# Optimization experiments

Hardware: AMD Instinct MI355X
Metric: run time of the kernel (lower is better)

The kernel has to match this reference:

```python
import jax, jax.numpy as jnp
import numpy as np

DIM = 64  # per-head dim; temperature init = sqrt(DIM)
B, H, S, D = 4, 12, 2048, 64


def setup_inputs() -> dict:
    key = jax.random.key(0)
    kq, kk, kv = jax.random.split(key, 3)
    Q = jax.random.normal(kq, (B, H, S, D), dtype=jnp.float32)
    K = jax.random.normal(kk, (B, H, S, D), dtype=jnp.float32)
    V = jax.random.normal(kv, (B, H, S, D), dtype=jnp.float32)
    temperature = jnp.ones((1,), dtype=jnp.float32) * (DIM ** 0.5)
    return {"Q": Q, "K": K, "V": V, "temperature": temperature}


def reference(Q, K, V, temperature):
    # scores: [B,H,S,S]
    scores = jnp.einsum("bhqd,bhkd->bhqk", Q, K) / temperature
    s = scores.shape[-1]
    eye = jnp.eye(s, dtype=bool)  # diagonal self-exclusion
    scores = jnp.where(eye, -jnp.inf, scores)
    attn = jax.nn.softmax(scores, axis=-1)
    return jnp.einsum("bhqk,bhkd->bhqd", attn, V)
```

## Files before the change

kernel.cpp:

```cpp
#include <hip/hip_runtime.h>
#include <hip/hip_bf16.h>

#define S_LEN 2048
#define D_DIM 64
#define NHEADS 48
#define QT 128
#define KT 64
#define NKT (S_LEN / KT)
#define HEAD_ELEMS ((size_t)S_LEN * D_DIM)
#define WS_NEED (3ull * NHEADS * S_LEN * D_DIM * 2ull)

typedef short bf16x8 __attribute__((ext_vector_type(8)));
typedef float f32x4 __attribute__((ext_vector_type(4)));

__device__ __forceinline__ unsigned short f2bf(float x) {
    unsigned u = __builtin_bit_cast(unsigned, x);
    u = (u + 0x7fffu + ((u >> 16) & 1u)) >> 16;
    return (unsigned short)u;
}

__device__ __forceinline__ unsigned cvtpk(float lo, float hi) {
    unsigned r;
    asm("v_cvt_pk_bf16_f32 %0, %1, %2" : "=v"(r) : "v"(lo), "v"(hi));
    return r;
}

__device__ __forceinline__ void gload16(const void* g, void* l) {
    __builtin_amdgcn_global_load_lds(
        (const __attribute__((address_space(1))) unsigned int*)g,
        (__attribute__((address_space(3))) unsigned int*)l, 16, 0, 0);
}

__global__ __launch_bounds__(256) void lsa_prep(
    const float* __restrict__ Qg, const float* __restrict__ Kg,
    const float* __restrict__ Vg, const float* __restrict__ Tg,
    unsigned short* __restrict__ Qs, unsigned short* __restrict__ Kf,
    unsigned short* __restrict__ Vf) {
    const int b   = blockIdx.x;
    const int tid = threadIdx.x;
    const int r   = tid >> 4;
    const int c4  = (tid & 15) * 4;

    __shared__ __align__(16) unsigned short Kl[4096];
    __shared__ __align__(16) unsigned short Vl[4096];

    const size_t ibase = (size_t)b * 4096;
    const float qscale = 1.442695041f / Tg[0];

#pragma unroll
    for (int it = 0; it < 4; ++it) {
        const int rr = it * 16 + r;
        const size_t off = ibase + (size_t)rr * D_DIM + c4;

        float4 q4 = *(const float4*)(Qg + off);
        uint2 qo;
        qo.x = cvtpk(q4.x * qscale, q4.y * qscale);
        qo.y = cvtpk(q4.z * qscale, q4.w * qscale);
        *(uint2*)&Qs[off] = qo;

        float4 k4 = *(const float4*)(Kg + off);
        {
            const int f = rr >> 4, l15 = rr & 15;
            const int c = c4 >> 5, lhi = (c4 >> 3) & 3, j0 = c4 & 7;
            uint2 ko;
            ko.x = cvtpk(k4.x, k4.y);
            ko.y = cvtpk(k4.z, k4.w);
            *(uint2*)&Kl[c * 2048 + f * 512 + ((lhi << 4) | l15) * 8 + j0] = ko;
        }

        float4 v4 = *(const float4*)(Vg + off);
        {
            const int cc = rr >> 5, rem = rr & 31;
            const int jv = ((rem >> 4) << 2) | (rem & 3);
            const int lhiv = (rem >> 2) & 3;
            const int g = c4 >> 4;
            const int base = cc * 2048 + g * 512 + (lhiv << 7) + jv;
            Vl[base + ((c4 + 0) & 15) * 8] = f2bf(v4.x);
            Vl[base + ((c4 + 1) & 15) * 8] = f2bf(v4.y);
            Vl[base + ((c4 + 2) & 15) * 8] = f2bf(v4.z);
            Vl[base + ((c4 + 3) & 15) * 8] = f2bf(v4.w);
        }
    }
    __syncthreads();
    const uint4* ks = (const uint4*)Kl;
    const uint4* vs = (const uint4*)Vl;
    uint4* kd = (uint4*)(Kf + ibase);
    uint4* vd = (uint4*)(Vf + ibase);
    kd[tid]       = ks[tid];
    kd[tid + 256] = ks[tid + 256];
    vd[tid]       = vs[tid];
    vd[tid + 256] = vs[tid + 256];
}

__global__ __launch_bounds__(256, 2) void lsa_attn_ns(
    const unsigned short* __restrict__ Qs, const unsigned short* __restrict__ Kf,
    const unsigned short* __restrict__ Vf, float* __restrict__ Og) {

    const int bid  = blockIdx.x;
    const int xcd  = bid & 7;
    const int idx  = bid >> 3;
    const int bh   = xcd * 6 + (idx >> 4);
    const int qt   = idx & 15;
    const int tid  = threadIdx.x;
    const int wid  = tid >> 6;
    const int lane = tid & 63;
    const int l15  = lane & 15;
    const int lhi  = lane >> 4;

    __shared__ __align__(16) unsigned short KV[2][2][KT * D_DIM];

    const unsigned short* Qh = Qs + (size_t)bh * HEAD_ELEMS;
    const char* Kh = (const char*)(Kf + (size_t)bh * HEAD_ELEMS);
    const char* Vh = (const char*)(Vf + (size_t)bh * HEAD_ELEMS);
    float* Ob = Og + (size_t)bh * HEAD_ELEMS;

    const int qbase   = qt * QT + wid * 32;
    const int diag_kt = qbase >> 6;

    bf16x8 qf[2][2];
#pragma unroll
    for (int rb = 0; rb < 2; ++rb) {
#pragma unroll
        for (int c = 0; c < 2; ++c) {
            qf[rb][c] = *(const bf16x8*)(Qh + (size_t)(qbase + rb * 16 + l15) * D_DIM
                                            + c * 32 + lhi * 8);
        }
    }

    const f32x4 zero4 = {0.f, 0.f, 0.f, 0.f};
    f32x4 acc[2][4];
    float lp[2];
#pragma unroll
    for (int rb = 0; rb < 2; ++rb) {
#pragma unroll
        for (int g = 0; g < 4; ++g) acc[rb][g] = zero4;
        lp[rb] = 0.f;
    }

    bf16x8 vr[8];
    f32x4 sf[2][4];
    bf16x8 pb[2][2];

#define ISSUE(BUF, T) do {                                                     \
    const char* ks_ = Kh + (size_t)(T) * 8192 + wid * 2048;                    \
    const char* vs_ = Vh + (size_t)(T) * 8192 + wid * 2048;                    \
    char* lk_ = (char*)&KV[BUF][0][0] + wid * 2048;                            \
    char* lv_ = (char*)&KV[BUF][1][0] + wid * 2048;                            \
    gload16(ks_ + lane * 16, lk_);                                             \
    gload16(ks_ + 1024 + lane * 16, lk_ + 1024);                               \
    gload16(vs_ + lane * 16, lv_);                                             \
    gload16(vs_ + 1024 + lane * 16, lv_ + 1024);                               \
} while (0)

#define DSQK(BUF) do {                                                         \
    const char* lk_ = (const char*)&KV[BUF][0][0] + lane * 16;                 \
    _Pragma("unroll")                                                          \
    for (int rb = 0; rb < 2; ++rb) {                                           \
        _Pragma("unroll")                                                      \
        for (int f = 0; f < 4; ++f) sf[rb][f] = zero4;                         \
    }                                                                          \
    _Pragma("unroll")                                                          \
    for (int c = 0; c < 2; ++c) {                                              \
        bf16x8 kb_[4];                                                         \
        _Pragma("unroll")                                                      \
        for (int f = 0; f < 4; ++f) {                                          \
            kb_[f] = *(const bf16x8*)(lk_ + c * 4096 + f * 1024);              \
        }                                                                      \
        __builtin_amdgcn_s_setprio(1);                                         \
        _Pragma("unroll")                                                      \
        for (int rb = 0; rb < 2; ++rb) {                                       \
            _Pragma("unroll")                                                  \
            for (int f = 0; f < 4; ++f) {                                      \
                sf[rb][f] = __builtin_amdgcn_mfma_f32_16x16x32_bf16(           \
                    kb_[f], qf[rb][c], sf[rb][f], 0, 0, 0);                    \
            }                                                                  \
        }                                                                      \
        __builtin_amdgcn_s_setprio(0);                                         \
    }                                                                          \
} while (0)

#define DSV(BUF) do {                                                          \
    const char* lv_ = (const char*)&KV[BUF][1][0] + lane * 16;                 \
    _Pragma("unroll")                                                          \
    for (int u = 0; u < 8; ++u) {                                              \
        vr[u] = *(const bf16x8*)(lv_ + (u >> 2) * 4096 + (u & 3) * 1024);      \
    }                                                                          \
} while (0)

#define PV() do {                                                              \
    __builtin_amdgcn_s_setprio(1);                                             \
    _Pragma("unroll")                                                          \
    for (int cc = 0; cc < 2; ++cc) {                                           \
        _Pragma("unroll")                                                      \
        for (int rb = 0; rb < 2; ++rb) {                                       \
            _Pragma("unroll")                                                  \
            for (int g = 0; g < 4; ++g) {                                      \
                acc[rb][g] = __builtin_amdgcn_mfma_f32_16x16x32_bf16(          \
                    vr[cc * 4 + g], pb[rb][cc], acc[rb][g], 0, 0, 0);          \
            }                                                                  \
        }                                                                      \
    }                                                                          \
    __builtin_amdgcn_s_setprio(0);                                             \
} while (0)

#define SMX(T) do {                                                            \
    if ((T) == diag_kt) {                                                      \
        _Pragma("unroll")                                                      \
        for (int rb = 0; rb < 2; ++rb) {                                       \
            const int q_ = qbase + rb * 16 + l15;                              \
            _Pragma("unroll")                                                  \
            for (int f = 0; f < 4; ++f) {                                      \
                _Pragma("unroll")                                              \
                for (int i = 0; i < 4; ++i) {                                  \
                    const int k_ = (T) * KT + f * 16 + lhi * 4 + i;            \
                    if (q_ == k_) sf[rb][f][i] = -1e30f;                       \
                }                                                              \
            }                                                                  \
        }                                                                      \
    }                                                                          \
    _Pragma("unroll")                                                          \
    for (int rb = 0; rb < 2; ++rb) {                                           \
        f32x4 ps_ = zero4;                                                     \
        _Pragma("unroll")                                                      \
        for (int f = 0; f < 4; ++f) {                                          \
            _Pragma("unroll")                                                  \
            for (int i = 0; i < 4; ++i) {                                      \
                sf[rb][f][i] = __builtin_amdgcn_exp2f(sf[rb][f][i]);           \
            }                                                                  \
            ps_ += sf[rb][f];                                                  \
        }                                                                      \
        lp[rb] += (ps_[0] + ps_[1]) + (ps_[2] + ps_[3]);                       \
        _Pragma("unroll")                                                      \
        for (int cc = 0; cc < 2; ++cc) {                                       \
            uint4 u_;                                                          \
            u_.x = cvtpk(sf[rb][cc * 2][0],     sf[rb][cc * 2][1]);            \
            u_.y = cvtpk(sf[rb][cc * 2][2],     sf[rb][cc * 2][3]);            \
            u_.z = cvtpk(sf[rb][cc * 2 + 1][0], sf[rb][cc * 2 + 1][1]);        \
            u_.w = cvtpk(sf[rb][cc * 2 + 1][2], sf[rb][cc * 2 + 1][3]);        \
            pb[rb][cc] = __builtin_bit_cast(bf16x8, u_);                       \
        }                                                                      \
    }                                                                          \
} while (0)

    ISSUE(0, 0);
    __syncthreads();
    ISSUE(1, 1);
    DSQK(0);
    DSV(0);

#pragma unroll 1
    for (int t = 0; t < NKT - 1; ++t) {
        SMX(t);
        PV();
        __syncthreads();
        if (t + 2 < NKT) ISSUE(t & 1, t + 2);
        DSQK((t + 1) & 1);
        DSV((t + 1) & 1);
    }
    SMX(NKT - 1);
    PV();

#undef ISSUE
#undef DSQK
#undef DSV
#undef PV
#undef SMX

#pragma unroll
    for (int rb = 0; rb < 2; ++rb) {
        float l = lp[rb];
        l += __shfl_xor(l, 16);
        l += __shfl_xor(l, 32);
        const float invl = 1.0f / l;
        const int q = qbase + rb * 16 + l15;
#pragma unroll
        for (int g = 0; g < 4; ++g) {
            float4 o;
            o.x = acc[rb][g][0] * invl;
            o.y = acc[rb][g][1] * invl;
            o.z = acc[rb][g][2] * invl;
            o.w = acc[rb][g][3] * invl;
            *(float4*)(Ob + (size_t)q * D_DIM + g * 16 + lhi * 4) = o;
        }
    }
}

__device__ __forceinline__ int swzK_fb(int row, int col) {
    return (row << 6) + (col ^ ((row & 7) << 3));
}
__device__ __forceinline__ int swzV_fb(int row, int col) {
    int f = (row ^ (row >> 3)) & 7;
    return (row << 6) + (col ^ (f << 3));
}

__global__ __launch_bounds__(256, 2) void lsa_attn_fb(
    const float* __restrict__ Qg, const float* __restrict__ Kg,
    const float* __restrict__ Vg, const float* __restrict__ Tg,
    float* __restrict__ Og) {

    const int bid  = blockIdx.x;
    const int bh   = bid >> 4;
    const int qt   = bid & 15;
    const int tid  = threadIdx.x;
    const int wid  = tid >> 6;
    const int lane = tid & 63;
    const int l15  = lane & 15;
    const int lhi  = lane >> 4;

    __shared__ __align__(16) unsigned short Kt[64 * D_DIM];
    __shared__ __align__(16) unsigned short Vt[D_DIM * 64];

    const size_t base = (size_t)bh * HEAD_ELEMS;
    const float* Qb = Qg + base;
    const float* Kb = Kg + base;
    const float* Vb = Vg + base;
    float*       Ob = Og + base;

    const float inv_t = 1.0f / Tg[0];
    const int qbase = qt * QT + wid * 32;
    const int diag_kt = qbase >> 6;

    bf16x8 qf[2][2];
#pragma unroll
    for (int rb = 0; rb < 2; ++rb) {
#pragma unroll
        for (int c = 0; c < 2; ++c) {
            const float* src = Qb + (size_t)(qbase + rb * 16 + l15) * D_DIM + c * 32 + lhi * 8;
            float4 a = *(const float4*)(src);
            float4 b = *(const float4*)(src + 4);
            bf16x8 v;
            v[0] = (short)f2bf(a.x * inv_t); v[1] = (short)f2bf(a.y * inv_t);
            v[2] = (short)f2bf(a.z * inv_t); v[3] = (short)f2bf(a.w * inv_t);
            v[4] = (short)f2bf(b.x * inv_t); v[5] = (short)f2bf(b.y * inv_t);
            v[6] = (short)f2bf(b.z * inv_t); v[7] = (short)f2bf(b.w * inv_t);
            qf[rb][c] = v;
        }
    }

    const f32x4 zero4 = {0.f, 0.f, 0.f, 0.f};
    f32x4 acc[2][4];
    float mrow[2], lrow[2];
#pragma unroll
    for (int rb = 0; rb < 2; ++rb) {
#pragma unroll
        for (int g = 0; g < 4; ++g) acc[rb][g] = zero4;
        mrow[rb] = -1e30f; lrow[rb] = 0.f;
    }

    const int ld_r = tid >> 4;
    const int ld_c = (tid & 15) * 4;
    float4 kreg[4], vreg[4];

#define LOAD_TILE(KT_IDX) do {                                                 \
    const int kb0_ = (KT_IDX) * 64;                                            \
    _Pragma("unroll")                                                          \
    for (int it = 0; it < 4; ++it) {                                           \
        const int r_ = it * 16 + ld_r;                                         \
        kreg[it] = *(const float4*)(Kb + (size_t)(kb0_ + r_) * D_DIM + ld_c);  \
        vreg[it] = *(const float4*)(Vb + (size_t)(kb0_ + r_) * D_DIM + ld_c);  \
    }                                                                          \
} while (0)

    LOAD_TILE(0);

    for (int kt = 0; kt < 32; ++kt) {
        const int kb0 = kt * 64;
        __syncthreads();
#pragma unroll
        for (int it = 0; it < 4; ++it) {
            const int r = it * 16 + ld_r;
            unsigned lo = (unsigned)f2bf(kreg[it].x) | ((unsigned)f2bf(kreg[it].y) << 16);
            unsigned hi = (unsigned)f2bf(kreg[it].z) | ((unsigned)f2bf(kreg[it].w) << 16);
            *(uint2*)&Kt[swzK_fb(r, ld_c)] = make_uint2(lo, hi);
            Vt[swzV_fb(ld_c + 0, r)] = f2bf(vreg[it].x);
            Vt[swzV_fb(ld_c + 1, r)] = f2bf(vreg[it].y);
            Vt[swzV_fb(ld_c + 2, r)] = f2bf(vreg[it].z);
            Vt[swzV_fb(ld_c + 3, r)] = f2bf(vreg[it].w);
        }
        __syncthreads();
        if (kt + 1 < 32) LOAD_TILE(kt + 1);

        f32x4 sf[2][4];
#pragma unroll
        for (int rb = 0; rb < 2; ++rb) {
#pragma unroll
            for (int f = 0; f < 4; ++f) sf[rb][f] = zero4;
        }

#pragma unroll
        for (int c = 0; c < 2; ++c) {
            bf16x8 kb[4];
#pragma unroll
            for (int f = 0; f < 4; ++f)
                kb[f] = *(const bf16x8*)&Kt[swzK_fb(f * 16 + l15, c * 32 + lhi * 8)];
#pragma unroll
            for (int rb = 0; rb < 2; ++rb) {
#pragma unroll
                for (int f = 0; f < 4; ++f)
                    sf[rb][f] = __builtin_amdgcn_mfma_f32_16x16x32_bf16(
                        kb[f], qf[rb][c], sf[rb][f], 0, 0, 0);
            }
        }

        if (kt == diag_kt) {
#pragma unroll
            for (int rb = 0; rb < 2; ++rb) {
                const int q = qbase + rb * 16 + l15;
#pragma unroll
                for (int f = 0; f < 4; ++f) {
#pragma unroll
                    for (int i = 0; i < 4; ++i) {
                        const int k = kb0 + f * 16 + lhi * 4 + i;
                        if (q == k) sf[rb][f][i] = -1e30f;
                    }
                }
            }
        }

        bf16x8 pb[2][2];
#pragma unroll
        for (int rb = 0; rb < 2; ++rb) {
            f32x4 mv;
#pragma unroll
            for (int i = 0; i < 4; ++i)
                mv[i] = fmaxf(fmaxf(sf[rb][0][i], sf[rb][1][i]),
                              fmaxf(sf[rb][2][i], sf[rb][3][i]));
            float m0 = fmaxf(fmaxf(mv[0], mv[1]), fmaxf(mv[2], mv[3]));
            m0 = fmaxf(m0, __shfl_xor(m0, 16));
            m0 = fmaxf(m0, __shfl_xor(m0, 32));
            const float mnew  = fmaxf(mrow[rb], m0);
            const float alpha = __expf(mrow[rb] - mnew);
            mrow[rb] = mnew;
            f32x4 ps = zero4;
#pragma unroll
            for (int f = 0; f < 4; ++f) {
#pragma unroll
                for (int i = 0; i < 4; ++i)
                    sf[rb][f][i] = __expf(sf[rb][f][i] - mnew);
                ps += sf[rb][f];
            }
            float s0 = (ps[0] + ps[1]) + (ps[2] + ps[3]);
            s0 += __shfl_xor(s0, 16);
            s0 += __shfl_xor(s0, 32);
            lrow[rb] = lrow[rb] * alpha + s0;
#pragma unroll
            for (int g = 0; g < 4; ++g) acc[rb][g] *= alpha;
#pragma unroll
            for (int cc = 0; cc < 2; ++cc) {
                bf16x8 v;
#pragma unroll
                for (int j = 0; j < 8; ++j)
                    v[j] = (short)f2bf(sf[rb][cc * 2 + (j >> 2)][j & 3]);
                pb[rb][cc] = v;
            }
        }

#pragma unroll
        for (int cc = 0; cc < 2; ++cc) {
            bf16x8 va[4];
#pragma unroll
            for (int g = 0; g < 4; ++g) {
                const int row = g * 16 + l15;
                uint2 lo = *(const uint2*)&Vt[swzV_fb(row, cc * 32 + lhi * 4)];
                uint2 hi = *(const uint2*)&Vt[swzV_fb(row, cc * 32 + 16 + lhi * 4)];
                bf16x8 t;
                ((uint2*)&t)[0] = lo;
                ((uint2*)&t)[1] = hi;
                va[g] = t;
            }
#pragma unroll
            for (int rb = 0; rb < 2; ++rb) {
#pragma unroll
                for (int g = 0; g < 4; ++g)
                    acc[rb][g] = __builtin_amdgcn_mfma_f32_16x16x32_bf16(
                        va[g], pb[rb][cc], acc[rb][g], 0, 0, 0);
            }
        }
    }
#undef LOAD_TILE

#pragma unroll
    for (int rb = 0; rb < 2; ++rb) {
        const float invl = 1.0f / lrow[rb];
        const int q = qbase + rb * 16 + l15;
#pragma unroll
        for (int g = 0; g < 4; ++g) {
            float4 o;
            o.x = acc[rb][g][0] * invl;
            o.y = acc[rb][g][1] * invl;
            o.z = acc[rb][g][2] * invl;
            o.w = acc[rb][g][3] * invl;
            *(float4*)(Ob + (size_t)q * D_DIM + g * 16 + lhi * 4) = o;
        }
    }
}

extern "C" void kernel_launch(void* const* d_in, const int* in_sizes, int n_in,
                              void* d_out, int out_size, void* d_ws, size_t ws_size,
                              hipStream_t stream) {
    const float* Q = (const float*)d_in[0];
    const float* K = (const float*)d_in[1];
    const float* V = (const float*)d_in[2];
    const float* T = (const float*)d_in[3];
    float* O = (float*)d_out;

    if (ws_size >= WS_NEED) {
        unsigned short* Qs = (unsigned short*)d_ws;
        unsigned short* Kf = Qs + NHEADS * HEAD_ELEMS;
        unsigned short* Vf = Kf + NHEADS * HEAD_ELEMS;
        hipLaunchKernelGGL(lsa_prep, dim3(NHEADS * NKT), dim3(256), 0, stream,
                           Q, K, V, T, Qs, Kf, Vf);
        hipLaunchKernelGGL(lsa_attn_ns, dim3(NHEADS * (S_LEN / QT)), dim3(256), 0, stream,
                           Qs, Kf, Vf, O);
    } else {
        hipLaunchKernelGGL(lsa_attn_fb, dim3(NHEADS * (S_LEN / QT)), dim3(256), 0, stream,
                           Q, K, V, T, O);
    }
}
```

Before: 76.34 us.

## Load two KV tiles per stage to halve barriers in attention loop

The K/V staging buffer now holds two 64-key tiles per double-buffer slot, so each async load stage fetches 128 keys and the main loop processes two tiles per iteration. This halves the number of __syncthreads barriers and load-issue points per block. It doubles LDS use per block to 64KB, which may limit occupancy at two blocks per CU, and it lengthens the prefetch distance.

```diff
diff --git a/kernel.cpp b/kernel.cpp
--- a/kernel.cpp
+++ b/kernel.cpp
@@ -7,6 +7,7 @@
 #define QT 128
 #define KT 64
 #define NKT (S_LEN / KT)
+#define NT2 (NKT / 2)
 #define HEAD_ELEMS ((size_t)S_LEN * D_DIM)
 #define WS_NEED (3ull * NHEADS * S_LEN * D_DIM * 2ull)
 
@@ -92,7 +93,7 @@
     vd[tid + 256] = vs[tid + 256];
 }
 
-__global__ __launch_bounds__(256, 2) void lsa_attn_ns(
+__global__ __launch_bounds__(256, 2) void lsa_attn_b2(
     const unsigned short* __restrict__ Qs, const unsigned short* __restrict__ Kf,
     const unsigned short* __restrict__ Vf, float* __restrict__ Og) {
 
@@ -107,7 +108,7 @@
     const int l15  = lane & 15;
     const int lhi  = lane >> 4;
 
-    __shared__ __align__(16) unsigned short KV[2][2][KT * D_DIM];
+    __shared__ __align__(16) unsigned short KV[2][2][2][KT * D_DIM];
 
     const unsigned short* Qh = Qs + (size_t)bh * HEAD_ELEMS;
     const char* Kh = (const char*)(Kf + (size_t)bh * HEAD_ELEMS);
@@ -141,19 +142,25 @@
     f32x4 sf[2][4];
     bf16x8 pb[2][2];
 
-#define ISSUE(BUF, T) do {                                                     \
-    const char* ks_ = Kh + (size_t)(T) * 8192 + wid * 2048;                    \
-    const char* vs_ = Vh + (size_t)(T) * 8192 + wid * 2048;                    \
-    char* lk_ = (char*)&KV[BUF][0][0] + wid * 2048;                            \
-    char* lv_ = (char*)&KV[BUF][1][0] + wid * 2048;                            \
-    gload16(ks_ + lane * 16, lk_);                                             \
-    gload16(ks_ + 1024 + lane * 16, lk_ + 1024);                               \
-    gload16(vs_ + lane * 16, lv_);                                             \
-    gload16(vs_ + 1024 + lane * 16, lv_ + 1024);                               \
+#define ISSUE(BUF, T2) do {                                                    \
+    const char* ks_ = Kh + (size_t)(T2) * 16384 + wid * 2048;                  \
+    const char* vs_ = Vh + (size_t)(T2) * 16384 + wid * 2048;                  \
+    char* lk0_ = (char*)&KV[BUF][0][0][0] + wid * 2048;                        \
+    char* lv0_ = (char*)&KV[BUF][0][1][0] + wid * 2048;                        \
+    char* lk1_ = (char*)&KV[BUF][1][0][0] + wid * 2048;                        \
+    char* lv1_ = (char*)&KV[BUF][1][1][0] + wid * 2048;                        \
+    gload16(ks_ + lane * 16, lk0_);                                            \
+    gload16(ks_ + 1024 + lane * 16, lk0_ + 1024);                              \
+    gload16(vs_ + lane * 16, lv0_);                                            \
+    gload16(vs_ + 1024 + lane * 16, lv0_ + 1024);                              \
+    gload16(ks_ + 8192 + lane * 16, lk1_);                                     \
+    gload16(ks_ + 9216 + lane * 16, lk1_ + 1024);                              \
+    gload16(vs_ + 8192 + lane * 16, lv1_);                                     \
+    gload16(vs_ + 9216 + lane * 16, lv1_ + 1024);                              \
 } while (0)
 
-#define DSQK(BUF) do {                                                         \
-    const char* lk_ = (const char*)&KV[BUF][0][0] + lane * 16;                 \
+#define DSQK(BUF, SUB) do {                                                    \
+    const char* lk_ = (const char*)&KV[BUF][SUB][0][0] + lane * 16;            \
     _Pragma("unroll")                                                          \
     for (int rb = 0; rb < 2; ++rb) {                                           \
         _Pragma("unroll")                                                      \
@@ -179,8 +186,8 @@
     }                                                                          \
 } while (0)
 
-#define DSV(BUF) do {                                                          \
-    const char* lv_ = (const char*)&KV[BUF][1][0] + lane * 16;                 \
+#define DSV(BUF, SUB) do {                                                     \
+    const char* lv_ = (const char*)&KV[BUF][SUB][1][0] + lane * 16;            \
     _Pragma("unroll")                                                          \
     for (int u = 0; u < 8; ++u) {                                              \
         vr[u] = *(const bf16x8*)(lv_ + (u >> 2) * 4096 + (u & 3) * 1024);      \
@@ -245,19 +252,27 @@
     ISSUE(0, 0);
     __syncthreads();
     ISSUE(1, 1);
-    DSQK(0);
-    DSV(0);
+    DSQK(0, 0);
+    DSV(0, 0);
 
 #pragma unroll 1
-    for (int t = 0; t < NKT - 1; ++t) {
-        SMX(t);
+    for (int t2 = 0; t2 < NT2 - 1; ++t2) {
+        SMX(2 * t2);
+        PV();
+        DSQK(t2 & 1, 1);
+        DSV(t2 & 1, 1);
+        SMX(2 * t2 + 1);
         PV();
         __syncthreads();
-        if (t + 2 < NKT) ISSUE(t & 1, t + 2);
-        DSQK((t + 1) & 1);
-        DSV((t + 1) & 1);
-    }
-    SMX(NKT - 1);
+        if (t2 + 2 < NT2) ISSUE(t2 & 1, t2 + 2);
+        DSQK((t2 + 1) & 1, 0);
+        DSV((t2 + 1) & 1, 0);
+    }
+    SMX(2 * (NT2 - 1));
+    PV();
+    DSQK((NT2 - 1) & 1, 1);
+    DSV((NT2 - 1) & 1, 1);
+    SMX(2 * NT2 - 1);
     PV();
 
 #undef ISSUE
@@ -510,7 +525,7 @@
         unsigned short* Vf = Kf + NHEADS * HEAD_ELEMS;
         hipLaunchKernelGGL(lsa_prep, dim3(NHEADS * NKT), dim3(256), 0, stream,
                            Q, K, V, T, Qs, Kf, Vf);
-        hipLaunchKernelGGL(lsa_attn_ns, dim3(NHEADS * (S_LEN / QT)), dim3(256), 0, stream,
+        hipLaunchKernelGGL(lsa_attn_b2, dim3(NHEADS * (S_LEN / QT)), dim3(256), 0, stream,
                            Qs, Kf, Vf, O);
     } else {
         hipLaunchKernelGGL(lsa_attn_fb, dim3(NHEADS * (S_LEN / QT)), dim3(256), 0, stream,
```

Result: slower. 78.46 us (+2.8%).
